# Kernel optimization log

Hardware: AMD Instinct MI355X
Metric: run time of the kernel (lower is better)

## Reference

```python
import jax, jax.numpy as jnp
import numpy as np

B, T, C, H = 2, 2048, 1024, 16
HD = C // H  # head dim = 64


def setup_inputs() -> dict:
    key = jax.random.key(0)
    ks = jax.random.split(key, 9)
    s = 1.0 / np.sqrt(C)
    return {
        "x": jax.random.normal(ks[0], (B, T, C), dtype=jnp.float32),
        "Wq": jax.random.normal(ks[1], (C, C), dtype=jnp.float32) * s,
        "bq": jax.random.normal(ks[2], (C,), dtype=jnp.float32) * 0.02,
        "Wk": jax.random.normal(ks[3], (C, C), dtype=jnp.float32) * s,
        "bk": jax.random.normal(ks[4], (C,), dtype=jnp.float32) * 0.02,
        "Wv": jax.random.normal(ks[5], (C, C), dtype=jnp.float32) * s,
        "bv": jax.random.normal(ks[6], (C,), dtype=jnp.float32) * 0.02,
        "Wo": jax.random.normal(ks[7], (C, C), dtype=jnp.float32) * s,
        "bo": jax.random.normal(ks[8], (C,), dtype=jnp.float32) * 0.02,
    }


def reference(x, Wq, bq, Wk, bk, Wv, bv, Wo, bo):
    # Projections (torch Linear: x @ W.T + b; here W stored pre-transposed as [C_in, C_out])
    q = x @ Wq + bq  # (B,T,C)
    k = x @ Wk + bk
    v = x @ Wv + bv
    # Split heads: (B,T,C) -> (B,H,T,HD)
    q = q.reshape(B, T, H, HD).transpose(0, 2, 1, 3)
    k = k.reshape(B, T, H, HD).transpose(0, 2, 1, 3)
    v = v.reshape(B, T, H, HD).transpose(0, 2, 1, 3)
    # NOTE: original module never applies a causal mask despite its name.
    score = jnp.einsum("bhqd,bhkd->bhqk", q, k) / jnp.sqrt(jnp.float32(HD))
    score = jax.nn.softmax(score, axis=-1)
    y = jnp.einsum("bhqk,bhkd->bhqd", score, v)
    y = y.transpose(0, 2, 1, 3).reshape(B, T, C)
    # dropout is identity in eval mode
    return y @ Wo + bo
```

## Files before the change

### kernel.cpp

```cpp
#include <hip/hip_runtime.h>
#include <math.h>

#define B_ 2
#define T_ 2048
#define C_ 1024
#define H_ 16
#define HD_ 64
#define M_ (B_*T_)

typedef _Float16 half2v __attribute__((ext_vector_type(2)));
typedef _Float16 half4v __attribute__((ext_vector_type(4)));
typedef _Float16 half8v __attribute__((ext_vector_type(8)));
typedef float f32x4 __attribute__((ext_vector_type(4)));

#define GLD_LDS(gp, lp) \
  __builtin_amdgcn_global_load_lds( \
      (const __attribute__((address_space(1))) void*)(gp), \
      (__attribute__((address_space(3))) void*)(lp), 16, 0, 0)

__global__ __launch_bounds__(256) void cast_f16_kernel(
    const float* __restrict__ src, _Float16* __restrict__ dst, int n4)
{
  int i = blockIdx.x * 256 + threadIdx.x;
  if (i < n4) {
    float4 v = ((const float4*)src)[i];
    half4v h; h[0] = (_Float16)v.x; h[1] = (_Float16)v.y;
    h[2] = (_Float16)v.z; h[3] = (_Float16)v.w;
    ((half4v*)dst)[i] = h;
  }
}

__global__ __launch_bounds__(256) void transpose_cast_all_kernel(
    const float* __restrict__ Wq, const float* __restrict__ Wk,
    const float* __restrict__ Wv, const float* __restrict__ Wo,
    _Float16* __restrict__ Wt3, _Float16* __restrict__ Wot)
{
  const float* W; _Float16* Wt;
  switch (blockIdx.z) {
    case 0:  W = Wq; Wt = Wt3; break;
    case 1:  W = Wk; Wt = Wt3 + (size_t)1024 * 1024; break;
    case 2:  W = Wv; Wt = Wt3 + (size_t)2048 * 1024; break;
    default: W = Wo; Wt = Wot; break;
  }
  __shared__ float tile[32][33];
  const int tx = threadIdx.x, ty = threadIdx.y;
  const int n0 = blockIdx.x * 32, k0 = blockIdx.y * 32;
#pragma unroll
  for (int r = 0; r < 4; r++) {
    int k = ty + r * 8;
    tile[k][tx] = W[(size_t)(k0 + k) * C_ + n0 + tx];
  }
  __syncthreads();
#pragma unroll
  for (int r = 0; r < 4; r++) {
    int n = ty + r * 8;
    Wt[(size_t)(n0 + n) * C_ + k0 + tx] = (_Float16)tile[tx][n];
  }
}

__global__ __launch_bounds__(256) void concat_bias_kernel(
    const float* __restrict__ bq, const float* __restrict__ bk,
    const float* __restrict__ bv, float* __restrict__ b3)
{
  int i = blockIdx.x * 256 + threadIdx.x;
  const float* s = (i < 1024) ? bq : ((i < 2048) ? bk : bv);
  b3[i] = s[i & 1023];
}

template <int BM, int BN, int EPI>
__global__ __launch_bounds__(256) void gemm_f16_kernel(
    const _Float16* __restrict__ A, const _Float16* __restrict__ Bw,
    const float* __restrict__ bias,
    _Float16* __restrict__ o0, _Float16* __restrict__ o1,
    _Float16* __restrict__ o2, float* __restrict__ of)
{
  constexpr int FM = BM / 32, FN = BN / 32;
  __shared__ __align__(16) _Float16 As[BM * 32];
  __shared__ __align__(16) _Float16 Bs[BN * 32];
  const int t = threadIdx.x;
  const int w = t >> 6, lane = t & 63, l15 = lane & 15, quad = lane >> 4;
  const int wm = (w & 1) * (BM / 2), wn = (w >> 1) * (BN / 2);
  const int bm = blockIdx.y * BM, bn = blockIdx.x * BN;
  const int lrow = lane >> 2, lcol = (lane & 3) * 8;

  f32x4 acc[FM][FN];
#pragma unroll
  for (int i = 0; i < FM; i++)
#pragma unroll
    for (int j = 0; j < FN; j++) acc[i][j] = (f32x4){0.f, 0.f, 0.f, 0.f};

  for (int k0 = 0; k0 < 1024; k0 += 32) {
#pragma unroll
    for (int i = 0; i < BM / 64; i++) {
      int ca = w + 4 * i;
      int row = ca * 16 + lrow;
      GLD_LDS(A + (size_t)(bm + row) * 1024 + k0 + lcol, As + ca * 512);
    }
#pragma unroll
    for (int i = 0; i < BN / 64; i++) {
      int cb = w + 4 * i;
      int row = cb * 16 + lrow;
      GLD_LDS(Bw + (size_t)(bn + row) * 1024 + k0 + lcol, Bs + cb * 512);
    }
    __syncthreads();

    half8v af[FM], bf[FN];
#pragma unroll
    for (int mt = 0; mt < FM; mt++)
      af[mt] = *(const half8v*)(As + (wm + mt * 16 + l15) * 32 + quad * 8);
#pragma unroll
    for (int nt = 0; nt < FN; nt++)
      bf[nt] = *(const half8v*)(Bs + (wn + nt * 16 + l15) * 32 + quad * 8);
#pragma unroll
    for (int mt = 0; mt < FM; mt++)
#pragma unroll
      for (int nt = 0; nt < FN; nt++)
        acc[mt][nt] = __builtin_amdgcn_mfma_f32_16x16x32_f16(
            af[mt], bf[nt], acc[mt][nt], 0, 0, 0);
    __syncthreads();
  }

#pragma unroll
  for (int mt = 0; mt < FM; mt++)
#pragma unroll
    for (int nt = 0; nt < FN; nt++) {
      int n = bn + wn + nt * 16 + l15;
      float bv = bias[n];
#pragma unroll
      for (int r = 0; r < 4; r++) {
        int m = bm + wm + mt * 16 + quad * 4 + r;
        float v = acc[mt][nt][r] + bv;
        if (EPI == 0) {
          if (bn < 1024) {
            o0[(size_t)m * 1024 + n] = (_Float16)(v * 0.180336884f);
          } else if (bn < 2048) {
            o1[(size_t)m * 1024 + (n - 1024)] = (_Float16)v;
          } else {
            int dg = n - 2048;
            int hh = dg >> 6, hd = dg & 63;
            int bb = m >> 11, tt = m & 2047;
            o2[(((size_t)(bb * H_ + hh)) * 64 + hd) * 2048 + tt] = (_Float16)v;
          }
        } else {
          of[(size_t)m * 1024 + n] = v;
        }
      }
    }
}

__global__ __launch_bounds__(256) void attn_f16_kernel(
    const _Float16* __restrict__ Qh, const _Float16* __restrict__ Kh,
    const _Float16* __restrict__ Vt, _Float16* __restrict__ Yh)
{
  __shared__ __align__(16) _Float16 Ks[64 * 68];
  __shared__ __align__(16) _Float16 Vs[64 * 68];
  const int t = threadIdx.x;
  const int w = t >> 6, lane = t & 63, l15 = lane & 15, quad = lane >> 4;
  const int qt = blockIdx.x, h = blockIdx.y, b = blockIdx.z;
  const int qg = qt * 64 + w * 16 + l15;
  const size_t qoff = ((size_t)(b * T_ + qg)) * C_ + h * HD_;

  half8v qf[2];
  qf[0] = *(const half8v*)(Qh + qoff + quad * 8);
  qf[1] = *(const half8v*)(Qh + qoff + 32 + quad * 8);

  f32x4 o[4];
#pragma unroll
  for (int i = 0; i < 4; i++) o[i] = (f32x4){0.f, 0.f, 0.f, 0.f};
  float m_run = -INFINITY, l_run = 0.f;

  const size_t kbase = ((size_t)b * T_) * C_ + h * HD_;
  const size_t vbase = ((size_t)(b * H_ + h)) * HD_ * 2048;

  const int srow = t >> 3, scp = t & 7;

  for (int kt0 = 0; kt0 < T_; kt0 += 64) {
#pragma unroll
    for (int i = 0; i < 2; i++) {
      int row = srow + i * 32;
      *(uint4*)((char*)Ks + row * 136 + scp * 16) =
          *(const uint4*)(Kh + kbase + (size_t)(kt0 + row) * C_ + scp * 8);
      *(uint4*)((char*)Vs + row * 136 + scp * 16) =
          *(const uint4*)(Vt + vbase + (size_t)row * 2048 + kt0 + scp * 8);
    }
    __syncthreads();

    f32x4 s[4];
#pragma unroll
    for (int kt = 0; kt < 4; kt++) {
      s[kt] = (f32x4){0.f, 0.f, 0.f, 0.f};
      int key = kt * 16 + l15;
#pragma unroll
      for (int ks = 0; ks < 2; ks++) {
        half8v kf = *(const half8v*)((char*)Ks + key * 136 + (ks * 4 + quad) * 16);
        s[kt] = __builtin_amdgcn_mfma_f32_16x16x32_f16(kf, qf[ks], s[kt], 0, 0, 0);
      }
    }

    float tmax = -INFINITY;
#pragma unroll
    for (int kt = 0; kt < 4; kt++)
#pragma unroll
      for (int r = 0; r < 4; r++) tmax = fmaxf(tmax, s[kt][r]);
    tmax = fmaxf(tmax, __shfl_xor(tmax, 16));
    tmax = fmaxf(tmax, __shfl_xor(tmax, 32));
    float mnew = fmaxf(m_run, tmax);
    float alpha = __builtin_amdgcn_exp2f(m_run - mnew);

    float psum = 0.f;
    half4v pf[4];
#pragma unroll
    for (int kt = 0; kt < 4; kt++) {
      float p0 = __builtin_amdgcn_exp2f(s[kt][0] - mnew);
      float p1 = __builtin_amdgcn_exp2f(s[kt][1] - mnew);
      float p2 = __builtin_amdgcn_exp2f(s[kt][2] - mnew);
      float p3 = __builtin_amdgcn_exp2f(s[kt][3] - mnew);
      psum += (p0 + p1) + (p2 + p3);
      half2v pk01 = __builtin_bit_cast(half2v, __builtin_amdgcn_cvt_pkrtz(p0, p1));
      half2v pk23 = __builtin_bit_cast(half2v, __builtin_amdgcn_cvt_pkrtz(p2, p3));
      pf[kt] = __builtin_shufflevector(pk01, pk23, 0, 1, 2, 3);
    }
    psum += __shfl_xor(psum, 16);
    psum += __shfl_xor(psum, 32);
    l_run = l_run * alpha + psum;
    m_run = mnew;
#pragma unroll
    for (int dt = 0; dt < 4; dt++) o[dt] *= alpha;

#pragma unroll
    for (int dt = 0; dt < 4; dt++) {
      int d = dt * 16 + l15;
#pragma unroll
      for (int kt = 0; kt < 4; kt++) {
        half4v vf = *(const half4v*)((char*)Vs + d * 136 + kt * 32 + quad * 8);
        o[dt] = __builtin_amdgcn_mfma_f32_16x16x16f16(vf, pf[kt], o[dt], 0, 0, 0);
      }
    }
    __syncthreads();
  }

  float inv = 1.0f / l_run;
#pragma unroll
  for (int dt = 0; dt < 4; dt++) {
    half4v yv;
#pragma unroll
    for (int r = 0; r < 4; r++) yv[r] = (_Float16)(o[dt][r] * inv);
    *(half4v*)(Yh + qoff + dt * 16 + quad * 4) = yv;
  }
}

extern "C" void kernel_launch(void* const* d_in, const int* in_sizes, int n_in,
                              void* d_out, int out_size, void* d_ws, size_t ws_size,
                              hipStream_t stream) {
  const float* x  = (const float*)d_in[0];
  const float* Wq = (const float*)d_in[1];
  const float* bq = (const float*)d_in[2];
  const float* Wk = (const float*)d_in[3];
  const float* bk = (const float*)d_in[4];
  const float* Wv = (const float*)d_in[5];
  const float* bv = (const float*)d_in[6];
  const float* Wo = (const float*)d_in[7];
  const float* bo = (const float*)d_in[8];
  float* out = (float*)d_out;

  char* ws = (char*)d_ws;
  _Float16* xh   = (_Float16*)(ws);
  _Float16* Qh   = (_Float16*)(ws + (((size_t)8)  << 20));
  _Float16* Kh   = (_Float16*)(ws + (((size_t)16) << 20));
  _Float16* Vt   = (_Float16*)(ws + (((size_t)24) << 20));
  _Float16* Yh   = (_Float16*)(ws + (((size_t)32) << 20));
  _Float16* Wt3  = (_Float16*)(ws + (((size_t)40) << 20));
  _Float16* Wot  = (_Float16*)(ws + (((size_t)46) << 20));
  float*    b3   = (float*)   (ws + (((size_t)48) << 20));

  cast_f16_kernel<<<(M_ * C_ / 4 + 255) / 256, 256, 0, stream>>>(x, xh, M_ * C_ / 4);
  transpose_cast_all_kernel<<<dim3(32, 32, 4), dim3(32, 8), 0, stream>>>(
      Wq, Wk, Wv, Wo, Wt3, Wot);
  concat_bias_kernel<<<12, 256, 0, stream>>>(bq, bk, bv, b3);

  gemm_f16_kernel<128, 128, 0><<<dim3(24, 32), 256, 0, stream>>>(
      xh, Wt3, b3, Qh, Kh, Vt, nullptr);

  attn_f16_kernel<<<dim3(T_ / 64, H_, B_), 256, 0, stream>>>(Qh, Kh, Vt, Yh);

  gemm_f16_kernel<64, 128, 1><<<dim3(8, 64), 256, 0, stream>>>(
      Yh, Wot, bo, nullptr, nullptr, nullptr, out);
}
```

Measured before the change: 223.1 us.

## Fuse prep kernels, double-buffer attention LDS, skip rescale when max unchanged

Merges the three preprocessing kernels (x cast, weight transpose-cast, bias concat) into one launch that dispatches on block index. In attention, K/V tiles go into two alternating LDS buffers so the trailing barrier can be dropped, and the global loads are issued together before the LDS stores. The online-softmax rescale of the output and running sum is skipped when no lane's tile max exceeds the running max. Together these cut launch overhead, one barrier per tile, and some exp/multiply work, at the cost of double the LDS per block and an extra branch.

After: 323.7 us. 45.1% more time.

```diff
diff --git a/kernel.cpp b/kernel.cpp
--- a/kernel.cpp
+++ b/kernel.cpp
@@ -18,53 +18,51 @@
       (const __attribute__((address_space(1))) void*)(gp), \
       (__attribute__((address_space(3))) void*)(lp), 16, 0, 0)
 
-__global__ __launch_bounds__(256) void cast_f16_kernel(
-    const float* __restrict__ src, _Float16* __restrict__ dst, int n4)
+__global__ __launch_bounds__(256) void prep_kernel(
+    const float* __restrict__ x,
+    const float* __restrict__ Wq, const float* __restrict__ Wk,
+    const float* __restrict__ Wv, const float* __restrict__ Wo,
+    const float* __restrict__ bq, const float* __restrict__ bk,
+    const float* __restrict__ bv,
+    _Float16* __restrict__ xh, _Float16* __restrict__ Wt3,
+    _Float16* __restrict__ Wot, float* __restrict__ b3)
 {
-  int i = blockIdx.x * 256 + threadIdx.x;
-  if (i < n4) {
-    float4 v = ((const float4*)src)[i];
+  __shared__ float tile[32][33];
+  const int blk = blockIdx.x, thr = threadIdx.x;
+  if (blk < 4096) {
+    int i = blk * 256 + thr;
+    float4 v = ((const float4*)x)[i];
     half4v h; h[0] = (_Float16)v.x; h[1] = (_Float16)v.y;
     h[2] = (_Float16)v.z; h[3] = (_Float16)v.w;
-    ((half4v*)dst)[i] = h;
-  }
-}
-
-__global__ __launch_bounds__(256) void transpose_cast_all_kernel(
-    const float* __restrict__ Wq, const float* __restrict__ Wk,
-    const float* __restrict__ Wv, const float* __restrict__ Wo,
-    _Float16* __restrict__ Wt3, _Float16* __restrict__ Wot)
-{
-  const float* W; _Float16* Wt;
-  switch (blockIdx.z) {
-    case 0:  W = Wq; Wt = Wt3; break;
-    case 1:  W = Wk; Wt = Wt3 + (size_t)1024 * 1024; break;
-    case 2:  W = Wv; Wt = Wt3 + (size_t)2048 * 1024; break;
-    default: W = Wo; Wt = Wot; break;
-  }
-  __shared__ float tile[32][33];
-  const int tx = threadIdx.x, ty = threadIdx.y;
-  const int n0 = blockIdx.x * 32, k0 = blockIdx.y * 32;
-#pragma unroll
-  for (int r = 0; r < 4; r++) {
-    int k = ty + r * 8;
-    tile[k][tx] = W[(size_t)(k0 + k) * C_ + n0 + tx];
-  }
-  __syncthreads();
-#pragma unroll
-  for (int r = 0; r < 4; r++) {
-    int n = ty + r * 8;
-    Wt[(size_t)(n0 + n) * C_ + k0 + tx] = (_Float16)tile[tx][n];
-  }
-}
-
-__global__ __launch_bounds__(256) void concat_bias_kernel(
-    const float* __restrict__ bq, const float* __restrict__ bk,
-    const float* __restrict__ bv, float* __restrict__ b3)
-{
-  int i = blockIdx.x * 256 + threadIdx.x;
-  const float* s = (i < 1024) ? bq : ((i < 2048) ? bk : bv);
-  b3[i] = s[i & 1023];
+    ((half4v*)xh)[i] = h;
+  } else if (blk < 8192) {
+    int zz = (blk - 4096) >> 10;
+    int bxy = (blk - 4096) & 1023;
+    const float* W; _Float16* Wt;
+    switch (zz) {
+      case 0:  W = Wq; Wt = Wt3; break;
+      case 1:  W = Wk; Wt = Wt3 + (size_t)1024 * 1024; break;
+      case 2:  W = Wv; Wt = Wt3 + (size_t)2048 * 1024; break;
+      default: W = Wo; Wt = Wot; break;
+    }
+    const int n0 = (bxy & 31) * 32, k0 = (bxy >> 5) * 32;
+    const int tx = thr & 31, ty = thr >> 5;
+#pragma unroll
+    for (int r = 0; r < 4; r++) {
+      int k = ty + r * 8;
+      tile[k][tx] = W[(size_t)(k0 + k) * C_ + n0 + tx];
+    }
+    __syncthreads();
+#pragma unroll
+    for (int r = 0; r < 4; r++) {
+      int n = ty + r * 8;
+      Wt[(size_t)(n0 + n) * C_ + k0 + tx] = (_Float16)tile[tx][n];
+    }
+  } else {
+    int i = (blk - 8192) * 256 + thr;
+    const float* s = (i < 1024) ? bq : ((i < 2048) ? bk : bv);
+    b3[i] = s[i & 1023];
+  }
 }
 
 template <int BM, int BN, int EPI>
@@ -152,8 +150,8 @@
     const _Float16* __restrict__ Qh, const _Float16* __restrict__ Kh,
     const _Float16* __restrict__ Vt, _Float16* __restrict__ Yh)
 {
-  __shared__ __align__(16) _Float16 Ks[64 * 68];
-  __shared__ __align__(16) _Float16 Vs[64 * 68];
+  __shared__ __align__(16) _Float16 Ks[2 * 64 * 68];
+  __shared__ __align__(16) _Float16 Vs[2 * 64 * 68];
   const int t = threadIdx.x;
   const int w = t >> 6, lane = t & 63, l15 = lane & 15, quad = lane >> 4;
   const int qt = blockIdx.x, h = blockIdx.y, b = blockIdx.z;
@@ -175,13 +173,19 @@
   const int srow = t >> 3, scp = t & 7;
 
   for (int kt0 = 0; kt0 < T_; kt0 += 64) {
-#pragma unroll
-    for (int i = 0; i < 2; i++) {
-      int row = srow + i * 32;
-      *(uint4*)((char*)Ks + row * 136 + scp * 16) =
-          *(const uint4*)(Kh + kbase + (size_t)(kt0 + row) * C_ + scp * 8);
-      *(uint4*)((char*)Vs + row * 136 + scp * 16) =
-          *(const uint4*)(Vt + vbase + (size_t)row * 2048 + kt0 + scp * 8);
+    const int cur = (kt0 >> 6) & 1;
+    char* Ksc = (char*)(Ks + cur * (64 * 68));
+    char* Vsc = (char*)(Vs + cur * (64 * 68));
+
+    {
+      uint4 k0v = *(const uint4*)(Kh + kbase + (size_t)(kt0 + srow) * C_ + scp * 8);
+      uint4 k1v = *(const uint4*)(Kh + kbase + (size_t)(kt0 + srow + 32) * C_ + scp * 8);
+      uint4 v0v = *(const uint4*)(Vt + vbase + (size_t)srow * 2048 + kt0 + scp * 8);
+      uint4 v1v = *(const uint4*)(Vt + vbase + (size_t)(srow + 32) * 2048 + kt0 + scp * 8);
+      *(uint4*)(Ksc + srow * 136 + scp * 16) = k0v;
+      *(uint4*)(Ksc + (srow + 32) * 136 + scp * 16) = k1v;
+      *(uint4*)(Vsc + srow * 136 + scp * 16) = v0v;
+      *(uint4*)(Vsc + (srow + 32) * 136 + scp * 16) = v1v;
     }
     __syncthreads();
 
@@ -192,7 +196,7 @@
       int key = kt * 16 + l15;
 #pragma unroll
       for (int ks = 0; ks < 2; ks++) {
-        half8v kf = *(const half8v*)((char*)Ks + key * 136 + (ks * 4 + quad) * 16);
+        half8v kf = *(const half8v*)(Ksc + key * 136 + (ks * 4 + quad) * 16);
         s[kt] = __builtin_amdgcn_mfma_f32_16x16x32_f16(kf, qf[ks], s[kt], 0, 0, 0);
       }
     }
@@ -204,17 +208,23 @@
       for (int r = 0; r < 4; r++) tmax = fmaxf(tmax, s[kt][r]);
     tmax = fmaxf(tmax, __shfl_xor(tmax, 16));
     tmax = fmaxf(tmax, __shfl_xor(tmax, 32));
-    float mnew = fmaxf(m_run, tmax);
-    float alpha = __builtin_amdgcn_exp2f(m_run - mnew);
+    if (__any(tmax > m_run)) {
+      float mnew = fmaxf(m_run, tmax);
+      float alpha = __builtin_amdgcn_exp2f(m_run - mnew);
+      l_run *= alpha;
+#pragma unroll
+      for (int dt = 0; dt < 4; dt++) o[dt] *= alpha;
+      m_run = mnew;
+    }
 
     float psum = 0.f;
     half4v pf[4];
 #pragma unroll
     for (int kt = 0; kt < 4; kt++) {
-      float p0 = __builtin_amdgcn_exp2f(s[kt][0] - mnew);
-      float p1 = __builtin_amdgcn_exp2f(s[kt][1] - mnew);
-      float p2 = __builtin_amdgcn_exp2f(s[kt][2] - mnew);
-      float p3 = __builtin_amdgcn_exp2f(s[kt][3] - mnew);
+      float p0 = __builtin_amdgcn_exp2f(s[kt][0] - m_run);
+      float p1 = __builtin_amdgcn_exp2f(s[kt][1] - m_run);
+      float p2 = __builtin_amdgcn_exp2f(s[kt][2] - m_run);
+      float p3 = __builtin_amdgcn_exp2f(s[kt][3] - m_run);
       psum += (p0 + p1) + (p2 + p3);
       half2v pk01 = __builtin_bit_cast(half2v, __builtin_amdgcn_cvt_pkrtz(p0, p1));
       half2v pk23 = __builtin_bit_cast(half2v, __builtin_amdgcn_cvt_pkrtz(p2, p3));
@@ -222,21 +232,17 @@
     }
     psum += __shfl_xor(psum, 16);
     psum += __shfl_xor(psum, 32);
-    l_run = l_run * alpha + psum;
-    m_run = mnew;
-#pragma unroll
-    for (int dt = 0; dt < 4; dt++) o[dt] *= alpha;
+    l_run += psum;
 
 #pragma unroll
     for (int dt = 0; dt < 4; dt++) {
       int d = dt * 16 + l15;
 #pragma unroll
       for (int kt = 0; kt < 4; kt++) {
-        half4v vf = *(const half4v*)((char*)Vs + d * 136 + kt * 32 + quad * 8);
+        half4v vf = *(const half4v*)(Vsc + d * 136 + kt * 32 + quad * 8);
         o[dt] = __builtin_amdgcn_mfma_f32_16x16x16f16(vf, pf[kt], o[dt], 0, 0, 0);
       }
     }
-    __syncthreads();
   }
 
   float inv = 1.0f / l_run;
@@ -273,10 +279,8 @@
   _Float16* Wot  = (_Float16*)(ws + (((size_t)46) << 20));
   float*    b3   = (float*)   (ws + (((size_t)48) << 20));
 
-  cast_f16_kernel<<<(M_ * C_ / 4 + 255) / 256, 256, 0, stream>>>(x, xh, M_ * C_ / 4);
-  transpose_cast_all_kernel<<<dim3(32, 32, 4), dim3(32, 8), 0, stream>>>(
-      Wq, Wk, Wv, Wo, Wt3, Wot);
-  concat_bias_kernel<<<12, 256, 0, stream>>>(bq, bk, bv, b3);
+  prep_kernel<<<8204, 256, 0, stream>>>(x, Wq, Wk, Wv, Wo, bq, bk, bv,
+                                        xh, Wt3, Wot, b3);
 
   gemm_f16_kernel<128, 128, 0><<<dim3(24, 32), 256, 0, stream>>>(
       xh, Wt3, b3, Qh, Kh, Vt, nullptr);
```
